# Performance work log

Hardware: AMD Instinct MI355X
Metric: run time of the kernel (lower is better)

The kernel has to match this reference:

```python
import jax, jax.numpy as jnp
import numpy as np

N, F, T, H, E = 50000, 16, 12, 64, 1600000
OUT = 1


def setup_inputs() -> dict:
    key = jax.random.key(0)
    ks = jax.random.split(key, 14)
    inp = {}
    inp["x"] = jax.random.normal(ks[0], (N, F, T), dtype=jnp.float32)
    inp["edge_index"] = jax.random.randint(ks[1], (2, E), 0, N, dtype=jnp.int32)
    inp["edge_weight"] = jax.random.uniform(ks[2], (E,), dtype=jnp.float32)
    C = F + H  # GCN input channels (x concat hidden)
    s = 0.05
    inp["Wz"] = jax.random.normal(ks[3], (C, H), dtype=jnp.float32) * s
    inp["bz"] = jnp.zeros((H,), dtype=jnp.float32)
    inp["Wr"] = jax.random.normal(ks[4], (C, H), dtype=jnp.float32) * s
    inp["br"] = jnp.zeros((H,), dtype=jnp.float32)
    inp["Wh"] = jax.random.normal(ks[5], (C, H), dtype=jnp.float32) * s
    inp["bh"] = jnp.zeros((H,), dtype=jnp.float32)
    inp["Wa"] = jax.random.normal(ks[6], (H, H), dtype=jnp.float32) * s
    inp["ba"] = jnp.zeros((H,), dtype=jnp.float32)
    inp["cv"] = jax.random.normal(ks[7], (H, 1), dtype=jnp.float32) * s
    inp["Wfc"] = jax.random.normal(ks[8], (H, OUT), dtype=jnp.float32) * s
    inp["bfc"] = jnp.zeros((OUT,), dtype=jnp.float32)
    return inp


def _gcn(xc, W, b, src, dst, ew_norm, self_norm, n):
    # PyG GCNConv: D^{-1/2}(A+I)D^{-1/2} X W + b, with self-loop weight 1
    xw = xc @ W                                   # [N, H]
    msg = xw[src] * ew_norm[:, None]              # [E, H] gather
    agg = jax.ops.segment_sum(msg, dst, num_segments=n)  # scatter-add
    return agg + self_norm[:, None] * xw + b


def reference(x, edge_index, edge_weight, Wz, bz, Wr, br, Wh, bh, Wa, ba, cv, Wfc, bfc):
    n = x.shape[0]
    src, dst = edge_index[0], edge_index[1]
    # symmetric normalization with self-loops (weight 1)
    deg = jax.ops.segment_sum(edge_weight, dst, num_segments=n) + 1.0
    dis = jax.lax.rsqrt(deg)
    ew_norm = dis[src] * edge_weight * dis[dst]
    self_norm = dis * dis

    x_seq = jnp.transpose(x, (2, 0, 1))  # [T, N, F]

    def step(h, x_t):
        xh = jnp.concatenate([x_t, h], axis=1)
        z = jax.nn.sigmoid(_gcn(xh, Wz, bz, src, dst, ew_norm, self_norm, n))
        r = jax.nn.sigmoid(_gcn(xh, Wr, br, src, dst, ew_norm, self_norm, n))
        xrh = jnp.concatenate([x_t, r * h], axis=1)
        hc = jnp.tanh(_gcn(xrh, Wh, bh, src, dst, ew_norm, self_norm, n))
        h_new = z * h + (1.0 - z) * hc
        return h_new, h_new

    h0 = jnp.zeros((n, Wz.shape[1]), dtype=x.dtype)
    _, hs_seq = jax.lax.scan(step, h0, x_seq)      # [T, N, H]

    hs_t = jnp.transpose(hs_seq, (1, 0, 2))        # [N, T, H]
    score = jnp.tanh(hs_t @ Wa + ba)               # [N, T, H]
    align = (score @ cv)[..., 0]                   # [N, T]
    alpha = jax.nn.softmax(align, axis=1)          # softmax over time
    context = jnp.einsum('nt,nth->nh', alpha, hs_t)
    out = context @ Wfc + bfc                      # [N, OUT]
    return out
```

## Files before the change

### kernel.cpp

```cpp
#include <hip/hip_runtime.h>
#include <hip/hip_fp16.h>
#include <math.h>

#define Nn 50000
#define Ff 16
#define Tt 12
#define Hh 64
#define Ee 1600000
#define Cc 80

#define SCAN_NB 98

typedef _Float16 f16x8 __attribute__((ext_vector_type(8)));
typedef float f32x4 __attribute__((ext_vector_type(4)));

static __device__ __forceinline__ float sigmoidf_(float x) { return 1.0f / (1.0f + expf(-x)); }

__global__ void k_deg(const int* __restrict__ ei, const float* __restrict__ ew,
                      unsigned long long* __restrict__ dc) {
  int e = blockIdx.x * blockDim.x + threadIdx.x;
  if (e >= Ee) return;
  int d = ei[Ee + e];
  unsigned long long pk = (1ULL << 42) + (unsigned long long)(ew[e] * 2097152.0f + 0.5f);
  atomicAdd(&dc[d], pk);
}

__global__ void k_dis(const unsigned long long* __restrict__ dc,
                      float* __restrict__ dis, int* __restrict__ cnt) {
  int i = blockIdx.x * blockDim.x + threadIdx.x;
  if (i >= Nn) return;
  unsigned long long v = dc[i];
  cnt[i] = (int)(v >> 42);
  float deg = (float)(v & ((1ULL << 42) - 1)) * (1.0f / 2097152.0f);
  dis[i] = 1.0f / sqrtf(deg + 1.0f);
}

__global__ __launch_bounds__(256) void k_scan1(const int* __restrict__ cnt,
                                               int* __restrict__ bsum) {
  __shared__ int ss[256];
  int b = blockIdx.x, t = threadIdx.x;
  int base = b * 512 + t * 2;
  int s = 0;
  if (base < Nn) s += cnt[base];
  if (base + 1 < Nn) s += cnt[base + 1];
  ss[t] = s;
  __syncthreads();
  for (int off = 128; off > 0; off >>= 1) {
    if (t < off) ss[t] += ss[t + off];
    __syncthreads();
  }
  if (t == 0) bsum[b] = ss[0];
}

__global__ __launch_bounds__(128) void k_scan2(const int* __restrict__ bsum,
                                               int* __restrict__ boff) {
  __shared__ int ss[128];
  int t = threadIdx.x;
  int v = (t < SCAN_NB) ? bsum[t] : 0;
  ss[t] = v;
  __syncthreads();
  for (int off = 1; off < 128; off <<= 1) {
    int u = (t >= off) ? ss[t - off] : 0;
    __syncthreads();
    ss[t] += u;
    __syncthreads();
  }
  if (t < SCAN_NB) boff[t] = ss[t] - v;
}

__global__ __launch_bounds__(256) void k_scan3(const int* __restrict__ cnt,
                                               const int* __restrict__ boff,
                                               int* __restrict__ rp, int* __restrict__ cur) {
  __shared__ int ss[256];
  int b = blockIdx.x, t = threadIdx.x;
  int base = b * 512 + t * 2;
  int c0 = (base < Nn) ? cnt[base] : 0;
  int c1 = (base + 1 < Nn) ? cnt[base + 1] : 0;
  int s = c0 + c1;
  ss[t] = s;
  __syncthreads();
  for (int off = 1; off < 256; off <<= 1) {
    int u = (t >= off) ? ss[t - off] : 0;
    __syncthreads();
    ss[t] += u;
    __syncthreads();
  }
  int run = boff[b] + ss[t] - s;
  if (base < Nn) { rp[base] = run; cur[base] = run; }
  if (base + 1 < Nn) { rp[base + 1] = run + c0; cur[base + 1] = run + c0; }
  if (b == 0 && t == 0) rp[Nn] = Ee;
}

__global__ void k_scatter(const int* __restrict__ ei, const float* __restrict__ ew,
                          const float* __restrict__ dis, int* __restrict__ cur,
                          int2* __restrict__ edge2) {
  int e = blockIdx.x * blockDim.x + threadIdx.x;
  if (e >= Ee) return;
  int s = ei[e];
  int d = ei[Ee + e];
  float w = ew[e] * dis[s] * dis[d];
  int pos = atomicAdd(&cur[d], 1);
  edge2[pos] = make_int2(s, __float_as_int(w));
}

__global__ void k_pack(const int2* __restrict__ edge2, unsigned* __restrict__ edge4) {
  int e = blockIdx.x * blockDim.x + threadIdx.x;
  if (e >= Ee) return;
  int2 v = edge2[e];
  __half wh = __float2half(__int_as_float(v.y));
  edge4[e] = (unsigned)(v.x & 0xFFFF) | ((unsigned)__half_as_ushort(wh) << 16);
}

__global__ void k_cvt_x(const float* __restrict__ x, __half* __restrict__ x16) {
  size_t idx = (size_t)blockIdx.x * blockDim.x + threadIdx.x;
  const size_t total = (size_t)Nn * Ff * Tt;
  if (idx < total) x16[idx] = __float2half(x[idx]);
}

__global__ void k_wfrag(const float* __restrict__ Wz, const float* __restrict__ Wr,
                        const float* __restrict__ Wh, __half* __restrict__ frag) {
  int t = blockIdx.x * 256 + threadIdx.x;
  if (t >= 12 * 3 * 64) return;
  int s = t / 192, rem = t % 192, ks = rem / 64, lane = rem % 64;
  int q = lane >> 4, nl = lane & 15;
  const float* W = (s < 4) ? Wz : (s < 8) ? Wr : Wh;
  int n0 = (s & 3) * 16;
  __half tmp[8];
#pragma unroll
  for (int j = 0; j < 8; j++) {
    int k = ks * 32 + q * 8 + j;
    float v = (k < Cc) ? W[k * Hh + n0 + nl] : 0.f;
    tmp[j] = __float2half(v);
  }
  *(uint4*)(frag + ((size_t)(s * 3 + ks) * 64 + lane) * 8) = *(uint4*)tmp;
}

__global__ void k_wfrag_a(const float* __restrict__ Wa, __half* __restrict__ fragA) {
  int t = blockIdx.x * 256 + threadIdx.x;
  if (t >= 8 * 64) return;
  int s = t >> 6, lane = t & 63;
  int tile = s >> 1, ks = s & 1;
  int q = lane >> 4, m = lane & 15;
  __half tmp[8];
#pragma unroll
  for (int j = 0; j < 8; j++) {
    int k = ks * 32 + q * 8 + j;
    tmp[j] = __float2half(Wa[k * Hh + tile * 16 + m]);
  }
  *(uint4*)(fragA + ((size_t)t) * 8) = *(uint4*)tmp;
}

__global__ __launch_bounds__(256) void k_agg_px(
    const float* __restrict__ x, const __half* __restrict__ x16, __half* __restrict__ Px16,
    const int* __restrict__ rp, const int2* __restrict__ edge2,
    const float* __restrict__ dis) {
  int i = blockIdx.x * 4 + (threadIdx.x >> 6);
  if (i >= Nn) return;
  int lane = threadIdx.x & 63;
  const int R = Ff * Tt;
  const bool act = lane < 48;
  float d = dis[i], sn = d * d;
  float a0 = 0.f, a1 = 0.f, a2 = 0.f, a3 = 0.f;
  if (act) {
    float4 sv = *(const float4*)(x + (size_t)i * R + 4 * lane);
    a0 = sn * sv.x; a1 = sn * sv.y; a2 = sn * sv.z; a3 = sn * sv.w;
  }
  int jb = rp[i], je = rp[i + 1];
  for (int j = jb; j < je; j += 2) {
    int jc1 = min(j + 1, Ee - 1);
    int2 e0 = edge2[j];
    int2 e1 = edge2[jc1];
    float w0 = __int_as_float(e0.y);
    float w1 = (j + 1 < je) ? __int_as_float(e1.y) : 0.f;
    if (act) {
      uint2 g0 = *(const uint2*)(x16 + (size_t)e0.x * R + 4 * lane);
      uint2 g1 = *(const uint2*)(x16 + (size_t)e1.x * R + 4 * lane);
      float2 p01 = __half22float2(*reinterpret_cast<const __half2*>(&g0.x));
      float2 p23 = __half22float2(*reinterpret_cast<const __half2*>(&g0.y));
      float2 q01 = __half22float2(*reinterpret_cast<const __half2*>(&g1.x));
      float2 q23 = __half22float2(*reinterpret_cast<const __half2*>(&g1.y));
      a0 = fmaf(w0, p01.x, a0); a1 = fmaf(w0, p01.y, a1);
      a2 = fmaf(w0, p23.x, a2); a3 = fmaf(w0, p23.y, a3);
      a0 = fmaf(w1, q01.x, a0); a1 = fmaf(w1, q01.y, a1);
      a2 = fmaf(w1, q23.x, a2); a3 = fmaf(w1, q23.y, a3);
    }
  }
  if (act) {
#pragma unroll
    for (int k = 0; k < 4; k++) {
      int cch = 4 * lane + k;
      int f = cch / Tt, tt = cch % Tt;
      float val = (k == 0) ? a0 : (k == 1) ? a1 : (k == 2) ? a2 : a3;
      Px16[(size_t)tt * Nn * Ff + (size_t)i * Ff + f] = __float2half(val);
    }
  }
}

static __device__ __forceinline__ void stage_px_zero(
    __half* sX16, const __half* __restrict__ Px16t, int i0, int tid) {
  if (tid < 32) {
    int n = tid >> 1, r = tid & 1;
    *(uint4*)(sX16 + n * 104 + r * 8) =
        *(const uint4*)(Px16t + (size_t)(i0 + n) * Ff + r * 8);
  } else if (tid < 80) {
    int p = tid - 32, n = p / 3, part = p % 3;
    *(uint4*)(sX16 + n * 104 + 80 + part * 8) = make_uint4(0u, 0u, 0u, 0u);
  }
}

static __device__ __forceinline__ void acc8_(const uint4& gv, float wt, float* a) {
  float2 f0 = __half22float2(*reinterpret_cast<const __half2*>(&gv.x));
  float2 f1 = __half22float2(*reinterpret_cast<const __half2*>(&gv.y));
  float2 f2 = __half22float2(*reinterpret_cast<const __half2*>(&gv.z));
  float2 f3 = __half22float2(*reinterpret_cast<const __half2*>(&gv.w));
  a[0] = fmaf(wt, f0.x, a[0]); a[1] = fmaf(wt, f0.y, a[1]);
  a[2] = fmaf(wt, f1.x, a[2]); a[3] = fmaf(wt, f1.y, a[3]);
  a[4] = fmaf(wt, f2.x, a[4]); a[5] = fmaf(wt, f2.y, a[5]);
  a[6] = fmaf(wt, f3.x, a[6]); a[7] = fmaf(wt, f3.y, a[7]);
}

static __device__ __forceinline__ void agg_node_to_lds(
    __half* sX16, int n, int i, int lane,
    const __half* __restrict__ v, const int* __restrict__ rp,
    const unsigned* __restrict__ edge4, const float* __restrict__ dis) {
  int g = lane >> 3;
  int c = lane & 7;
  float d = dis[i], sn = d * d;
  float a[8];
  {
    uint4 gv = *(const uint4*)(v + (size_t)i * Hh + 8 * c);
    float ws = (g == 0) ? sn : 0.f;
    float2 f0 = __half22float2(*reinterpret_cast<const __half2*>(&gv.x));
    float2 f1 = __half22float2(*reinterpret_cast<const __half2*>(&gv.y));
    float2 f2 = __half22float2(*reinterpret_cast<const __half2*>(&gv.z));
    float2 f3 = __half22float2(*reinterpret_cast<const __half2*>(&gv.w));
    a[0] = ws * f0.x; a[1] = ws * f0.y; a[2] = ws * f1.x; a[3] = ws * f1.y;
    a[4] = ws * f2.x; a[5] = ws * f2.y; a[6] = ws * f3.x; a[7] = ws * f3.y;
  }
  int jb = rp[i], je = rp[i + 1];
  for (int j0 = jb; j0 < je; j0 += 32) {
    int j1 = j0 + g, j2 = j0 + 8 + g, j3 = j0 + 16 + g, j4 = j0 + 24 + g;
    unsigned e1 = edge4[min(j1, Ee - 1)];
    unsigned e2 = edge4[min(j2, Ee - 1)];
    unsigned e3 = edge4[min(j3, Ee - 1)];
    unsigned e4 = edge4[min(j4, Ee - 1)];
    float w1 = (j1 < je) ? __half2float(__ushort_as_half((unsigned short)(e1 >> 16))) : 0.f;
    float w2 = (j2 < je) ? __half2float(__ushort_as_half((unsigned short)(e2 >> 16))) : 0.f;
    float w3 = (j3 < je) ? __half2float(__ushort_as_half((unsigned short)(e3 >> 16))) : 0.f;
    float w4 = (j4 < je) ? __half2float(__ushort_as_half((unsigned short)(e4 >> 16))) : 0.f;
    uint4 g1 = *(const uint4*)(v + (size_t)(e1 & 0xFFFFu) * Hh + 8 * c);
    uint4 g2 = *(const uint4*)(v + (size_t)(e2 & 0xFFFFu) * Hh + 8 * c);
    uint4 g3 = *(const uint4*)(v + (size_t)(e3 & 0xFFFFu) * Hh + 8 * c);
    uint4 g4 = *(const uint4*)(v + (size_t)(e4 & 0xFFFFu) * Hh + 8 * c);
    acc8_(g1, w1, a);
    acc8_(g2, w2, a);
    acc8_(g3, w3, a);
    acc8_(g4, w4, a);
  }
#pragma unroll
  for (int k2 = 0; k2 < 8; k2++) {
    a[k2] += __shfl_xor(a[k2], 8, 64);
    a[k2] += __shfl_xor(a[k2], 16, 64);
    a[k2] += __shfl_xor(a[k2], 32, 64);
  }
  if (g == 0) {
    __half2 h0 = __floats2half2_rn(a[0], a[1]);
    __half2 h1 = __floats2half2_rn(a[2], a[3]);
    __half2 h2 = __floats2half2_rn(a[4], a[5]);
    __half2 h3 = __floats2half2_rn(a[6], a[7]);
    uint4 st;
    st.x = *reinterpret_cast<unsigned int*>(&h0);
    st.y = *reinterpret_cast<unsigned int*>(&h1);
    st.z = *reinterpret_cast<unsigned int*>(&h2);
    st.w = *reinterpret_cast<unsigned int*>(&h3);
    *(uint4*)(sX16 + n * 104 + 16 + 8 * c) = st;
  }
}

__global__ __launch_bounds__(256) void k_zr_f(
    const __half* __restrict__ Px16, const __half* __restrict__ h16,
    const __half* __restrict__ frag,
    const float* __restrict__ bz, const float* __restrict__ br,
    const int* __restrict__ rp, const unsigned* __restrict__ edge4,
    const float* __restrict__ dis,
    __half* __restrict__ zb16, __half* __restrict__ rh16, int tstep) {
  __shared__ __align__(16) __half sX16[16 * 104];
  const int tid = threadIdx.x;
  const int i0 = blockIdx.x * 16;
  const int wv = tid >> 6, lane = tid & 63;
  f16x8 bzf[3], brf[3];
#pragma unroll
  for (int ks = 0; ks < 3; ks++) {
    bzf[ks] = *(const f16x8*)(frag + ((size_t)(wv * 3 + ks) * 64 + lane) * 8);
    brf[ks] = *(const f16x8*)(frag + ((size_t)((4 + wv) * 3 + ks) * 64 + lane) * 8);
  }
  stage_px_zero(sX16, Px16 + (size_t)tstep * Nn * Ff, i0, tid);
#pragma unroll
  for (int k = 0; k < 4; k++) {
    int n = wv * 4 + k;
    agg_node_to_lds(sX16, n, i0 + n, lane, h16, rp, edge4, dis);
  }
  __syncthreads();
  const int m = lane & 15, q = lane >> 4;
  f32x4 accz = {0.f, 0.f, 0.f, 0.f}, accr = {0.f, 0.f, 0.f, 0.f};
#pragma unroll
  for (int ks = 0; ks < 3; ks++) {
    f16x8 a = *(const f16x8*)(sX16 + m * 104 + ks * 32 + q * 8);
    accz = __builtin_amdgcn_mfma_f32_16x16x32_f16(a, bzf[ks], accz, 0, 0, 0);
    accr = __builtin_amdgcn_mfma_f32_16x16x32_f16(a, brf[ks], accr, 0, 0, 0);
  }
  const int o = wv * 16 + m;
  float bzo = bz[o], bro = br[o];
  const int nb = i0 + q * 4;
#pragma unroll
  for (int r = 0; r < 4; r++) {
    int node = nb + r;
    float zv = sigmoidf_(accz[r] + bzo);
    float rv = sigmoidf_(accr[r] + bro);
    float hv = __half2float(h16[(size_t)node * Hh + o]);
    zb16[(size_t)node * Hh + o] = __float2half(zv);
    rh16[(size_t)node * Hh + o] = __float2half(rv * hv);
  }
}

__global__ __launch_bounds__(256) void k_h_f(
    const __half* __restrict__ Px16, const __half* __restrict__ rh16,
    const __half* __restrict__ zb16, float* __restrict__ h, __half* __restrict__ h16,
    __half* __restrict__ hs16, const __half* __restrict__ frag,
    const float* __restrict__ bh,
    const int* __restrict__ rp, const unsigned* __restrict__ edge4,
    const float* __restrict__ dis, int tstep) {
  __shared__ __align__(16) __half sX16[16 * 104];
  const int tid = threadIdx.x;
  const int i0 = blockIdx.x * 16;
  const int wv = tid >> 6, lane = tid & 63;
  f16x8 bf[3];
#pragma unroll
  for (int ks = 0; ks < 3; ks++)
    bf[ks] = *(const f16x8*)(frag + ((size_t)((8 + wv) * 3 + ks) * 64 + lane) * 8);
  stage_px_zero(sX16, Px16 + (size_t)tstep * Nn * Ff, i0, tid);
#pragma unroll
  for (int k = 0; k < 4; k++) {
    int n = wv * 4 + k;
    agg_node_to_lds(sX16, n, i0 + n, lane, rh16, rp, edge4, dis);
  }
  __syncthreads();
  const int m = lane & 15, q = lane >> 4;
  f32x4 acc = {0.f, 0.f, 0.f, 0.f};
#pragma unroll
  for (int ks = 0; ks < 3; ks++) {
    f16x8 a = *(const f16x8*)(sX16 + m * 104 + ks * 32 + q * 8);
    acc = __builtin_amdgcn_mfma_f32_16x16x32_f16(a, bf[ks], acc, 0, 0, 0);
  }
  const int o = wv * 16 + m;
  float bho = bh[o];
  const int nb = i0 + q * 4;
  __half* hst = hs16 + (size_t)tstep * Nn * Hh;
#pragma unroll
  for (int r = 0; r < 4; r++) {
    int node = nb + r;
    float hc = tanhf(acc[r] + bho);
    float zv = __half2float(zb16[(size_t)node * Hh + o]);
    float hv = h[(size_t)node * Hh + o];
    float hn = zv * hv + (1.0f - zv) * hc;
    h[(size_t)node * Hh + o] = hn;
    __half hh = __float2half(hn);
    h16[(size_t)node * Hh + o] = hh;
    hst[(size_t)node * Hh + o] = hh;
  }
}

__global__ __launch_bounds__(256) void k_att(
    const __half* __restrict__ hs16, const __half* __restrict__ fragA,
    const float* __restrict__ ba, const float* __restrict__ cv,
    const float* __restrict__ Wfc, const float* __restrict__ bfc,
    float* __restrict__ out) {
  const int tid = threadIdx.x;
  const int wv = tid >> 6, lane = tid & 63;
  const int i = blockIdx.x * 4 + wv;
  if (i >= Nn) return;
  const int m = lane & 15, q = lane >> 4;

  f16x8 bf[4][2];
#pragma unroll
  for (int s = 0; s < 8; s++)
    bf[s >> 1][s & 1] = *(const f16x8*)(fragA + (size_t)(s * 64 + lane) * 8);

  const int tm = (m < Tt) ? m : (Tt - 1);
  const __half* hbase = hs16 + (size_t)tm * Nn * Hh + (size_t)i * Hh;
  f16x8 a0 = *(const f16x8*)(hbase + q * 8);
  f16x8 a1 = *(const f16x8*)(hbase + 32 + q * 8);

  f32x4 acc[4];
#pragma unroll
  for (int tile = 0; tile < 4; tile++) acc[tile] = f32x4{0.f, 0.f, 0.f, 0.f};
#pragma unroll
  for (int tile = 0; tile < 4; tile++) {
    acc[tile] = __builtin_amdgcn_mfma_f32_16x16x32_f16(a0, bf[tile][0], acc[tile], 0, 0, 0);
    acc[tile] = __builtin_amdgcn_mfma_f32_16x16x32_f16(a1, bf[tile][1], acc[tile], 0, 0, 0);
  }

  float ba_l[4], cv_l[4];
#pragma unroll
  for (int tile = 0; tile < 4; tile++) {
    ba_l[tile] = ba[tile * 16 + m];
    cv_l[tile] = cv[tile * 16 + m];
  }
  float ar[4];
#pragma unroll
  for (int r = 0; r < 4; r++) {
    float s = 0.f;
#pragma unroll
    for (int tile = 0; tile < 4; tile++)
      s += tanhf(acc[tile][r] + ba_l[tile]) * cv_l[tile];
    s += __shfl_xor(s, 1, 64);
    s += __shfl_xor(s, 2, 64);
    s += __shfl_xor(s, 4, 64);
    s += __shfl_xor(s, 8, 64);
    ar[r] = s;
  }
  float al[Tt];
#pragma unroll
  for (int t = 0; t < Tt; t++) al[t] = __shfl(ar[t & 3], (t >> 2) * 16, 64);
  float mx = al[0];
#pragma unroll
  for (int t = 1; t < Tt; t++) mx = fmaxf(mx, al[t]);
  float ssum = 0.f;
#pragma unroll
  for (int t = 0; t < Tt; t++) { al[t] = expf(al[t] - mx); ssum += al[t]; }
  float inv = 1.0f / ssum;
  float cx = 0.f;
#pragma unroll
  for (int t = 0; t < Tt; t++)
    cx = fmaf(al[t], __half2float(hs16[(size_t)t * Nn * Hh + (size_t)i * Hh + lane]), cx);
  float p = cx * inv * Wfc[lane];
#pragma unroll
  for (int off = 32; off >= 1; off >>= 1) p += __shfl_xor(p, off, 64);
  if (lane == 0) out[i] = p + bfc[0];
}

extern "C" void kernel_launch(void* const* d_in, const int* in_sizes, int n_in,
                              void* d_out, int out_size, void* d_ws, size_t ws_size,
                              hipStream_t stream) {
  const float* x   = (const float*)d_in[0];
  const int* ei    = (const int*)d_in[1];
  const float* ew  = (const float*)d_in[2];
  const float* Wz  = (const float*)d_in[3];
  const float* bz  = (const float*)d_in[4];
  const float* Wr  = (const float*)d_in[5];
  const float* br  = (const float*)d_in[6];
  const float* Wh  = (const float*)d_in[7];
  const float* bh  = (const float*)d_in[8];
  const float* Wa  = (const float*)d_in[9];
  const float* ba  = (const float*)d_in[10];
  const float* cv  = (const float*)d_in[11];
  const float* Wfc = (const float*)d_in[12];
  const float* bfc = (const float*)d_in[13];
  float* out = (float*)d_out;

  char* w = (char*)d_ws;
  auto alloc = [&](size_t bytes) {
    char* p = w;
    w += (bytes + 255) & ~(size_t)255;
    return p;
  };
  unsigned long long* dc = (unsigned long long*)alloc((size_t)Nn * 8);
  float* dis = (float*)alloc((size_t)Nn * 4);
  int* cnt   = (int*)alloc((size_t)Nn * 4);
  int* rp    = (int*)alloc((size_t)(Nn + 1) * 4);
  int* cur   = (int*)alloc((size_t)Nn * 4);
  int* bsum  = (int*)alloc((size_t)SCAN_NB * 4);
  int* boff  = (int*)alloc((size_t)SCAN_NB * 4);
  int2* edge2 = (int2*)alloc((size_t)Ee * 8);
  unsigned* edge4 = (unsigned*)alloc((size_t)Ee * 4);
  __half* x16  = (__half*)alloc((size_t)Nn * Ff * Tt * 2);
  __half* Px16 = (__half*)alloc((size_t)Tt * Nn * Ff * 2);
  float* h     = (float*)alloc((size_t)Nn * Hh * 4);
  __half* h16  = (__half*)alloc((size_t)Nn * Hh * 2);
  __half* rh16 = (__half*)alloc((size_t)Nn * Hh * 2);
  __half* zb16 = (__half*)alloc((size_t)Nn * Hh * 2);
  __half* hs16 = (__half*)alloc((size_t)Tt * Nn * Hh * 2);
  __half* wfrag = (__half*)alloc((size_t)12 * 3 * 64 * 8 * 2);
  __half* wfragA = (__half*)alloc((size_t)8 * 64 * 8 * 2);

  hipMemsetAsync(dc, 0, (size_t)Nn * 8, stream);
  hipMemsetAsync(h, 0, (size_t)Nn * Hh * 4, stream);
  hipMemsetAsync(h16, 0, (size_t)Nn * Hh * 2, stream);

  k_deg<<<(Ee + 255) / 256, 256, 0, stream>>>(ei, ew, dc);
  k_dis<<<(Nn + 255) / 256, 256, 0, stream>>>(dc, dis, cnt);
  k_scan1<<<SCAN_NB, 256, 0, stream>>>(cnt, bsum);
  k_scan2<<<1, 128, 0, stream>>>(bsum, boff);
  k_scan3<<<SCAN_NB, 256, 0, stream>>>(cnt, boff, rp, cur);
  k_scatter<<<(Ee + 255) / 256, 256, 0, stream>>>(ei, ew, dis, cur, edge2);
  k_pack<<<(Ee + 255) / 256, 256, 0, stream>>>(edge2, edge4);
  {
    const size_t total = (size_t)Nn * Ff * Tt;
    k_cvt_x<<<(int)((total + 255) / 256), 256, 0, stream>>>(x, x16);
  }
  k_wfrag<<<9, 256, 0, stream>>>(Wz, Wr, Wh, wfrag);
  k_wfrag_a<<<2, 256, 0, stream>>>(Wa, wfragA);
  k_agg_px<<<(Nn + 3) / 4, 256, 0, stream>>>(x, x16, Px16, rp, edge2, dis);

  const int gGemm = Nn / 16;
  const int gNode = (Nn + 3) / 4;
  for (int t = 0; t < Tt; t++) {
    k_zr_f<<<gGemm, 256, 0, stream>>>(Px16, h16, wfrag, bz, br, rp, edge4, dis,
                                      zb16, rh16, t);
    k_h_f<<<gGemm, 256, 0, stream>>>(Px16, rh16, zb16, h, h16, hs16, wfrag, bh,
                                     rp, edge4, dis, t);
  }
  k_att<<<gNode, 256, 0, stream>>>(hs16, wfragA, ba, cv, Wfc, bfc, out);
}
```

Measured before the change: 1.403 ms.

## Split graph aggregation into separate kernel over half-split hidden layout

Result: slower. 1.614 ms (+15.0%).

```diff
diff --git a/kernel.cpp b/kernel.cpp
--- a/kernel.cpp
+++ b/kernel.cpp
@@ -196,18 +196,6 @@
   }
 }
 
-static __device__ __forceinline__ void stage_px_zero(
-    __half* sX16, const __half* __restrict__ Px16t, int i0, int tid) {
-  if (tid < 32) {
-    int n = tid >> 1, r = tid & 1;
-    *(uint4*)(sX16 + n * 104 + r * 8) =
-        *(const uint4*)(Px16t + (size_t)(i0 + n) * Ff + r * 8);
-  } else if (tid < 80) {
-    int p = tid - 32, n = p / 3, part = p % 3;
-    *(uint4*)(sX16 + n * 104 + 80 + part * 8) = make_uint4(0u, 0u, 0u, 0u);
-  }
-}
-
 static __device__ __forceinline__ void acc8_(const uint4& gv, float wt, float* a) {
   float2 f0 = __half22float2(*reinterpret_cast<const __half2*>(&gv.x));
   float2 f1 = __half22float2(*reinterpret_cast<const __half2*>(&gv.y));
@@ -219,16 +207,22 @@
   a[6] = fmaf(wt, f3.x, a[6]); a[7] = fmaf(wt, f3.y, a[7]);
 }
 
-static __device__ __forceinline__ void agg_node_to_lds(
-    __half* sX16, int n, int i, int lane,
-    const __half* __restrict__ v, const int* __restrict__ rp,
-    const unsigned* __restrict__ edge4, const float* __restrict__ dis) {
-  int g = lane >> 3;
-  int c = lane & 7;
+__global__ __launch_bounds__(256) void k_agg2h(
+    const __half* __restrict__ vhs, __half* __restrict__ outs,
+    const int* __restrict__ rp, const unsigned* __restrict__ edge4,
+    const float* __restrict__ dis) {
+  const int b = blockIdx.x;
+  const int wv = threadIdx.x >> 6, lane = threadIdx.x & 63;
+  const int hf = b & 1;
+  const int i = (b >> 1) * 4 + wv;
+  if (i >= Nn) return;
+  const __half* vp = vhs + (size_t)hf * Nn * 32;
+  const int g = lane >> 2;
+  const int c = lane & 3;
   float d = dis[i], sn = d * d;
   float a[8];
   {
-    uint4 gv = *(const uint4*)(v + (size_t)i * Hh + 8 * c);
+    uint4 gv = *(const uint4*)(vp + (size_t)i * 32 + 8 * c);
     float ws = (g == 0) ? sn : 0.f;
     float2 f0 = __half22float2(*reinterpret_cast<const __half2*>(&gv.x));
     float2 f1 = __half22float2(*reinterpret_cast<const __half2*>(&gv.y));
@@ -239,26 +233,19 @@
   }
   int jb = rp[i], je = rp[i + 1];
   for (int j0 = jb; j0 < je; j0 += 32) {
-    int j1 = j0 + g, j2 = j0 + 8 + g, j3 = j0 + 16 + g, j4 = j0 + 24 + g;
+    int j1 = j0 + g, j2 = j0 + 16 + g;
     unsigned e1 = edge4[min(j1, Ee - 1)];
     unsigned e2 = edge4[min(j2, Ee - 1)];
-    unsigned e3 = edge4[min(j3, Ee - 1)];
-    unsigned e4 = edge4[min(j4, Ee - 1)];
     float w1 = (j1 < je) ? __half2float(__ushort_as_half((unsigned short)(e1 >> 16))) : 0.f;
     float w2 = (j2 < je) ? __half2float(__ushort_as_half((unsigned short)(e2 >> 16))) : 0.f;
-    float w3 = (j3 < je) ? __half2float(__ushort_as_half((unsigned short)(e3 >> 16))) : 0.f;
-    float w4 = (j4 < je) ? __half2float(__ushort_as_half((unsigned short)(e4 >> 16))) : 0.f;
-    uint4 g1 = *(const uint4*)(v + (size_t)(e1 & 0xFFFFu) * Hh + 8 * c);
-    uint4 g2 = *(const uint4*)(v + (size_t)(e2 & 0xFFFFu) * Hh + 8 * c);
-    uint4 g3 = *(const uint4*)(v + (size_t)(e3 & 0xFFFFu) * Hh + 8 * c);
-    uint4 g4 = *(const uint4*)(v + (size_t)(e4 & 0xFFFFu) * Hh + 8 * c);
+    uint4 g1 = *(const uint4*)(vp + (size_t)(e1 & 0xFFFFu) * 32 + 8 * c);
+    uint4 g2 = *(const uint4*)(vp + (size_t)(e2 & 0xFFFFu) * 32 + 8 * c);
     acc8_(g1, w1, a);
     acc8_(g2, w2, a);
-    acc8_(g3, w3, a);
-    acc8_(g4, w4, a);
   }
 #pragma unroll
   for (int k2 = 0; k2 < 8; k2++) {
+    a[k2] += __shfl_xor(a[k2], 4, 64);
     a[k2] += __shfl_xor(a[k2], 8, 64);
     a[k2] += __shfl_xor(a[k2], 16, 64);
     a[k2] += __shfl_xor(a[k2], 32, 64);
@@ -273,17 +260,33 @@
     st.y = *reinterpret_cast<unsigned int*>(&h1);
     st.z = *reinterpret_cast<unsigned int*>(&h2);
     st.w = *reinterpret_cast<unsigned int*>(&h3);
-    *(uint4*)(sX16 + n * 104 + 16 + 8 * c) = st;
-  }
-}
-
-__global__ __launch_bounds__(256) void k_zr_f(
-    const __half* __restrict__ Px16, const __half* __restrict__ h16,
-    const __half* __restrict__ frag,
+    *(uint4*)(outs + (size_t)hf * Nn * 32 + (size_t)i * 32 + 8 * c) = st;
+  }
+}
+
+static __device__ __forceinline__ void stage_px_pagg_zero(
+    __half* sX16, const __half* __restrict__ Px16t, const __half* __restrict__ Pagg,
+    int i0, int tid) {
+  if (tid < 32) {
+    int n = tid >> 1, r = tid & 1;
+    *(uint4*)(sX16 + n * 104 + r * 8) =
+        *(const uint4*)(Px16t + (size_t)(i0 + n) * Ff + r * 8);
+  } else if (tid < 160) {
+    int u = tid - 32, n = u >> 3, part = u & 7;
+    const __half* src = Pagg + (part >= 4 ? (size_t)Nn * 32 : 0) +
+                        (size_t)(i0 + n) * 32 + (part & 3) * 8;
+    *(uint4*)(sX16 + n * 104 + 16 + part * 8) = *(const uint4*)src;
+  } else if (tid < 208) {
+    int p = tid - 160, n = p / 3, part = p % 3;
+    *(uint4*)(sX16 + n * 104 + 80 + part * 8) = make_uint4(0u, 0u, 0u, 0u);
+  }
+}
+
+__global__ __launch_bounds__(256) void k_gemm_zr(
+    const __half* __restrict__ Px16, const __half* __restrict__ Pagg,
+    const __half* __restrict__ h16s, const __half* __restrict__ frag,
     const float* __restrict__ bz, const float* __restrict__ br,
-    const int* __restrict__ rp, const unsigned* __restrict__ edge4,
-    const float* __restrict__ dis,
-    __half* __restrict__ zb16, __half* __restrict__ rh16, int tstep) {
+    __half* __restrict__ zb16, __half* __restrict__ rh16s, int tstep) {
   __shared__ __align__(16) __half sX16[16 * 104];
   const int tid = threadIdx.x;
   const int i0 = blockIdx.x * 16;
@@ -294,12 +297,7 @@
     bzf[ks] = *(const f16x8*)(frag + ((size_t)(wv * 3 + ks) * 64 + lane) * 8);
     brf[ks] = *(const f16x8*)(frag + ((size_t)((4 + wv) * 3 + ks) * 64 + lane) * 8);
   }
-  stage_px_zero(sX16, Px16 + (size_t)tstep * Nn * Ff, i0, tid);
-#pragma unroll
-  for (int k = 0; k < 4; k++) {
-    int n = wv * 4 + k;
-    agg_node_to_lds(sX16, n, i0 + n, lane, h16, rp, edge4, dis);
-  }
+  stage_px_pagg_zero(sX16, Px16 + (size_t)tstep * Nn * Ff, Pagg, i0, tid);
   __syncthreads();
   const int m = lane & 15, q = lane >> 4;
   f32x4 accz = {0.f, 0.f, 0.f, 0.f}, accr = {0.f, 0.f, 0.f, 0.f};
@@ -312,24 +310,24 @@
   const int o = wv * 16 + m;
   float bzo = bz[o], bro = br[o];
   const int nb = i0 + q * 4;
+  const size_t po = (size_t)(o >> 5) * Nn * 32;
+  const int oc = o & 31;
 #pragma unroll
   for (int r = 0; r < 4; r++) {
     int node = nb + r;
     float zv = sigmoidf_(accz[r] + bzo);
     float rv = sigmoidf_(accr[r] + bro);
-    float hv = __half2float(h16[(size_t)node * Hh + o]);
+    float hv = __half2float(h16s[po + (size_t)node * 32 + oc]);
     zb16[(size_t)node * Hh + o] = __float2half(zv);
-    rh16[(size_t)node * Hh + o] = __float2half(rv * hv);
-  }
-}
-
-__global__ __launch_bounds__(256) void k_h_f(
-    const __half* __restrict__ Px16, const __half* __restrict__ rh16,
-    const __half* __restrict__ zb16, float* __restrict__ h, __half* __restrict__ h16,
+    rh16s[po + (size_t)node * 32 + oc] = __float2half(rv * hv);
+  }
+}
+
+__global__ __launch_bounds__(256) void k_gemm_h(
+    const __half* __restrict__ Px16, const __half* __restrict__ Pagg,
+    const __half* __restrict__ zb16, float* __restrict__ h, __half* __restrict__ h16s,
     __half* __restrict__ hs16, const __half* __restrict__ frag,
-    const float* __restrict__ bh,
-    const int* __restrict__ rp, const unsigned* __restrict__ edge4,
-    const float* __restrict__ dis, int tstep) {
+    const float* __restrict__ bh, int tstep) {
   __shared__ __align__(16) __half sX16[16 * 104];
   const int tid = threadIdx.x;
   const int i0 = blockIdx.x * 16;
@@ -338,12 +336,7 @@
 #pragma unroll
   for (int ks = 0; ks < 3; ks++)
     bf[ks] = *(const f16x8*)(frag + ((size_t)((8 + wv) * 3 + ks) * 64 + lane) * 8);
-  stage_px_zero(sX16, Px16 + (size_t)tstep * Nn * Ff, i0, tid);
-#pragma unroll
-  for (int k = 0; k < 4; k++) {
-    int n = wv * 4 + k;
-    agg_node_to_lds(sX16, n, i0 + n, lane, rh16, rp, edge4, dis);
-  }
+  stage_px_pagg_zero(sX16, Px16 + (size_t)tstep * Nn * Ff, Pagg, i0, tid);
   __syncthreads();
   const int m = lane & 15, q = lane >> 4;
   f32x4 acc = {0.f, 0.f, 0.f, 0.f};
@@ -356,6 +349,8 @@
   float bho = bh[o];
   const int nb = i0 + q * 4;
   __half* hst = hs16 + (size_t)tstep * Nn * Hh;
+  const size_t po = (size_t)(o >> 5) * Nn * 32;
+  const int oc = o & 31;
 #pragma unroll
   for (int r = 0; r < 4; r++) {
     int node = nb + r;
@@ -365,7 +360,7 @@
     float hn = zv * hv + (1.0f - zv) * hc;
     h[(size_t)node * Hh + o] = hn;
     __half hh = __float2half(hn);
-    h16[(size_t)node * Hh + o] = hh;
+    h16s[po + (size_t)node * 32 + oc] = hh;
     hst[(size_t)node * Hh + o] = hh;
   }
 }
@@ -476,16 +471,17 @@
   __half* x16  = (__half*)alloc((size_t)Nn * Ff * Tt * 2);
   __half* Px16 = (__half*)alloc((size_t)Tt * Nn * Ff * 2);
   float* h     = (float*)alloc((size_t)Nn * Hh * 4);
-  __half* h16  = (__half*)alloc((size_t)Nn * Hh * 2);
-  __half* rh16 = (__half*)alloc((size_t)Nn * Hh * 2);
+  __half* h16s  = (__half*)alloc((size_t)2 * Nn * 32 * 2);
+  __half* rh16s = (__half*)alloc((size_t)2 * Nn * 32 * 2);
   __half* zb16 = (__half*)alloc((size_t)Nn * Hh * 2);
+  __half* Pagg = (__half*)alloc((size_t)2 * Nn * 32 * 2);
   __half* hs16 = (__half*)alloc((size_t)Tt * Nn * Hh * 2);
   __half* wfrag = (__half*)alloc((size_t)12 * 3 * 64 * 8 * 2);
   __half* wfragA = (__half*)alloc((size_t)8 * 64 * 8 * 2);
 
   hipMemsetAsync(dc, 0, (size_t)Nn * 8, stream);
   hipMemsetAsync(h, 0, (size_t)Nn * Hh * 4, stream);
-  hipMemsetAsync(h16, 0, (size_t)Nn * Hh * 2, stream);
+  hipMemsetAsync(h16s, 0, (size_t)2 * Nn * 32 * 2, stream);
 
   k_deg<<<(Ee + 255) / 256, 256, 0, stream>>>(ei, ew, dc);
   k_dis<<<(Nn + 255) / 256, 256, 0, stream>>>(dc, dis, cnt);
@@ -503,12 +499,14 @@
   k_agg_px<<<(Nn + 3) / 4, 256, 0, stream>>>(x, x16, Px16, rp, edge2, dis);
 
   const int gGemm = Nn / 16;
+  const int gAgg = (Nn / 4) * 2;
   const int gNode = (Nn + 3) / 4;
   for (int t = 0; t < Tt; t++) {
-    k_zr_f<<<gGemm, 256, 0, stream>>>(Px16, h16, wfrag, bz, br, rp, edge4, dis,
-                                      zb16, rh16, t);
-    k_h_f<<<gGemm, 256, 0, stream>>>(Px16, rh16, zb16, h, h16, hs16, wfrag, bh,
-                                     rp, edge4, dis, t);
+    k_agg2h<<<gAgg, 256, 0, stream>>>(h16s, Pagg, rp, edge4, dis);
+    k_gemm_zr<<<gGemm, 256, 0, stream>>>(Px16, Pagg, h16s, wfrag, bz, br,
+                                         zb16, rh16s, t);
+    k_agg2h<<<gAgg, 256, 0, stream>>>(rh16s, Pagg, rp, edge4, dis);
+    k_gemm_h<<<gGemm, 256, 0, stream>>>(Px16, Pagg, zb16, h, h16s, hs16, wfrag, bh, t);
   }
   k_att<<<gNode, 256, 0, stream>>>(hs16, wfragA, ba, cv, Wfc, bfc, out);
 }
```
